# Performance work log

Measured on AMD Instinct MI355X. Metric: run time of the kernel, lower is better.

The kernel has to match this reference:

```python
import jax, jax.numpy as jnp
import numpy as np

SR = 16000
NYQ = SR / 2.0
N_FFT = 400
HOP = 160
WIN = 400
OUT_CHANNELS = 64
OUTPUT_SIZE = 64
MIN_LOW_HZ = 50.0
MIN_BAND_HZ = 50.0
FRAME_LENGTH = 400
EPS_LN = 1e-5


def _to_mel(hz):
    return 2595.0 * np.log10(1.0 + hz / 700.0)


def _to_hz(mel):
    return 700.0 * (10.0 ** (mel / 2595.0) - 1.0)


def setup_inputs() -> dict:
    key = jax.random.key(0)
    k1, = jax.random.split(key, 1)
    waveforms = jax.random.normal(k1, (1024, 1, 16000), dtype=jnp.float32)
    # mel-spaced init, exactly as in __init__ (freq_init='mel', range_constraint=False)
    low_hz = 30.0
    high_hz = NYQ - (MIN_LOW_HZ + MIN_BAND_HZ)
    mel = np.linspace(_to_mel(low_hz), _to_mel(high_hz), OUT_CHANNELS + 1)
    hz = _to_hz(mel)
    low_hz_ = jnp.asarray(hz[:-1], dtype=jnp.float32).reshape(-1, 1)
    band_hz_ = jnp.asarray(np.diff(hz), dtype=jnp.float32).reshape(-1, 1)
    ln_weight = jnp.ones((OUT_CHANNELS, 1), dtype=jnp.float32)
    ln_bias = jnp.zeros((OUT_CHANNELS, 1), dtype=jnp.float32)
    return {
        "waveforms": waveforms,
        "low_hz_": low_hz_,
        "band_hz_": band_hz_,
        "ln_weight": ln_weight,
        "ln_bias": ln_bias,
    }


def _hann_periodic(n):
    # torch.hann_window default: periodic=True
    k = jnp.arange(n, dtype=jnp.float32)
    return 0.5 - 0.5 * jnp.cos(2.0 * jnp.pi * k / n)


def _stft_mag(x):
    pad = N_FFT // 2
    xp = jnp.pad(x, ((0, 0), (pad, pad)), mode="reflect")
    n_frames = 1 + (xp.shape[1] - N_FFT) // HOP
    idx = jnp.arange(n_frames)[:, None] * HOP + jnp.arange(N_FFT)[None, :]
    frames = xp[:, idx] * _hann_periodic(WIN)  # [B, F_t, n_fft]
    spec = jnp.fft.rfft(frames, axis=-1)       # [B, F_t, n_fft//2+1]
    return jnp.abs(spec).transpose(0, 2, 1)    # [B, n_fft//2+1, F_t]


def _get_filters(low_hz_, band_hz_):
    # vectorized over all channels (original loops per channel)
    low = MIN_LOW_HZ + jnp.abs(low_hz_)                                   # [C,1]
    high = jnp.clip(low + MIN_BAND_HZ + jnp.abs(band_hz_), MIN_LOW_HZ, NYQ)
    freq = jnp.linspace(0.0, NYQ, N_FFT // 2 + 1, dtype=jnp.float32)      # [F]
    mask = (freq >= low) & (freq <= high)                                 # [C,F]
    center = (low + high) / 2.0
    bw = high - low
    resp = 1.0 - jnp.abs(freq - center) / (bw / 2.0)                      # triangular
    return jnp.where(mask, resp, 0.0)                                     # [C,F]


def _gln(x, weight, bias):
    # GlobalLayerNorm over dims (1,2) of [B,C,T]
    mean = jnp.mean(x, axis=(1, 2), keepdims=True)
    var = jnp.mean((x - mean) ** 2, axis=(1, 2), keepdims=True)
    return weight * (x - mean) / jnp.sqrt(var + EPS_LN) + bias


def _interp_linear(x, out_size):
    # torch F.interpolate(mode='linear', align_corners=False) along last dim
    t_in = x.shape[-1]
    scale = t_in / out_size
    pos = (jnp.arange(out_size, dtype=jnp.float32) + 0.5) * scale - 0.5
    pos = jnp.clip(pos, 0.0, t_in - 1)
    i0 = jnp.floor(pos).astype(jnp.int32)
    i1 = jnp.minimum(i0 + 1, t_in - 1)
    w = (pos - i0.astype(jnp.float32))
    return x[..., i0] * (1.0 - w) + x[..., i1] * w


def reference(waveforms, low_hz_, band_hz_, ln_weight, ln_bias):
    B = waveforms.shape[0]
    target_length = HOP * (OUTPUT_SIZE - 1) + FRAME_LENGTH  # 10480
    cur = waveforms.shape[-1]
    x = waveforms[:, 0, :]
    if target_length > cur:  # static shape decision
        x = jnp.pad(x, ((0, 0), (0, target_length - cur)))
    mag_spec = _stft_mag(x)                       # [B, 201, F_t]
    filters = _get_filters(low_hz_, band_hz_)     # [C, 201]
    filtered = jnp.einsum("cf,bft->bct", filters, mag_spec)  # [B, C, F_t]
    filtered = _gln(filtered, ln_weight, ln_bias)
    energy = filtered ** 2
    log_energy = jnp.log10(energy + 1e-6)         # [B, C, F_t]
    if log_energy.shape[-1] != OUTPUT_SIZE:
        log_energy = _interp_linear(log_energy, OUTPUT_SIZE)  # [B, C, 64]
    log_energy = log_energy[:, None, :, :].transpose(0, 1, 3, 2)  # [B,1,64,C]
    return (log_energy, filters)
```

## Files before the change

kernel.cpp:

```cpp
#include <hip/hip_runtime.h>
#include <math.h>

#define BLOCK 1024
#define MSTR 209

typedef __attribute__((ext_vector_type(8))) short short8;
typedef __attribute__((ext_vector_type(16))) float f32x16;
typedef __attribute__((ext_vector_type(8))) float f32x8;

__device__ inline unsigned short f2bf(float x) {
    unsigned u = __float_as_uint(x);
    unsigned r = u + 0x7fffu + ((u >> 16) & 1u);
    return (unsigned short)(r >> 16);
}

struct ASplit { short8 h, l; };

__device__ inline ASplit splitA_fast(f32x8 v) {
    unsigned h[4], l[4];
    #pragma unroll
    for (int q = 0; q < 4; ++q) {
        unsigned u0 = __float_as_uint(v[2*q]);
        unsigned u1 = __float_as_uint(v[2*q+1]);
        h[q] = __builtin_amdgcn_perm(u1, u0, 0x07060302u);
        float r0 = v[2*q]   - __uint_as_float(u0 & 0xFFFF0000u);
        float r1 = v[2*q+1] - __uint_as_float(u1 & 0xFFFF0000u);
        l[q] = __builtin_amdgcn_perm(__float_as_uint(r1), __float_as_uint(r0), 0x07060302u);
    }
    ASplit r;
    r.h = __builtin_bit_cast(short8, *(uint4*)h);
    r.l = __builtin_bit_cast(short8, *(uint4*)l);
    return r;
}

__device__ inline f32x8 loadA8(const float* __restrict__ x, int i0) {
    f32x8 r;
    if (i0 >= 0 && i0 <= 15992) {
        float4 a0 = *(const float4*)(x + i0);
        float4 a1 = *(const float4*)(x + i0 + 4);
        r[0] = a0.x; r[1] = a0.y; r[2] = a0.z; r[3] = a0.w;
        r[4] = a1.x; r[5] = a1.y; r[6] = a1.z; r[7] = a1.w;
    } else {
        #pragma unroll
        for (int e = 0; e < 8; ++e) {
            int p = i0 + e;
            p = (p < 0) ? -p : p;
            p = (p > 15999) ? (31998 - p) : p;
            r[e] = x[p];
        }
    }
    return r;
}

__device__ inline void filter_params(int c, const float* low_hz_, const float* band_hz_,
                                     float* fctr, float* finv, int* fks, int* fke) {
    float lo = 50.0f + fabsf(low_hz_[c]);
    float hi = lo + 50.0f + fabsf(band_hz_[c]);
    hi = fminf(fmaxf(hi, 50.0f), 8000.0f);
    float ctr = 0.5f * (lo + hi);
    float hbw = 0.5f * (hi - lo);
    int ks = (int)ceilf(lo * 0.025f);
    if (ks < 0) ks = 0;
    while (40.0f * (float)ks < lo) ++ks;
    while (ks > 0 && 40.0f * (float)(ks - 1) >= lo) --ks;
    int ke = (int)floorf(hi * 0.025f);
    if (ke > 200) ke = 200;
    while (40.0f * (float)ke > hi) --ke;
    while (ke < 200 && 40.0f * (float)(ke + 1) <= hi) ++ke;
    fctr[c] = ctr;
    finv[c] = (hbw > 0.0f) ? (1.0f / hbw) : 0.0f;
    fks[c]  = ks;
    fke[c]  = ke;
}

__global__ void fse_filters(const float* __restrict__ low_hz_,
                            const float* __restrict__ band_hz_,
                            float* __restrict__ out)
{
    int idx = blockIdx.x * 256 + threadIdx.x;
    if (idx >= 64 * 201) return;
    int c = idx / 201;
    int k = idx - c * 201;
    float lo = 50.0f + fabsf(low_hz_[c]);
    float hi = lo + 50.0f + fabsf(band_hz_[c]);
    hi = fminf(fmaxf(hi, 50.0f), 8000.0f);
    float ctr = 0.5f * (lo + hi);
    float hbw = 0.5f * (hi - lo);
    float fq = 40.0f * (float)k;
    float resp = 1.0f - fabsf(fq - ctr) / hbw;
    out[idx] = (fq >= lo && fq <= hi) ? resp : 0.0f;
}

__global__ void fse_setup_B(unsigned short* __restrict__ bt)
{
    int idx = blockIdx.x * 256 + threadIdx.x;
    if (idx >= 372736) return;
    int e   = idx & 7;
    int t   = idx >> 3;
    int row = t % 448;
    int q   = t / 448;
    int p   = q & 3;
    int pl  = (q >> 2) & 1;
    int kc  = q >> 3;
    int n   = kc * 32 + p * 8 + e;
    float v = 0.0f;
    if (n < 400) {
        int bin = -1, isim = 0;
        if (row <= 200) bin = row;
        else if (row >= 224 && row <= 424) { bin = row - 224; isim = 1; }
        if (bin >= 0) {
            int a = (bin * n) % 400;
            float th = 6.283185307179586f * ((float)a / 400.0f);
            float sn, cs;
            sincosf(th, &sn, &cs);
            float wn = 0.5f - 0.5f * cosf(6.283185307179586f * ((float)n / 400.0f));
            v = isim ? (-wn * sn) : (wn * cs);
        }
    }
    unsigned short h = f2bf(v);
    float hf = __uint_as_float((unsigned)h << 16);
    unsigned short l = f2bf(v - hf);
    bt[idx] = pl ? l : h;
}

#define KSTEP(KC, CUROFF, A0c, A1c, A0n, A1n, PRE)                            \
  {                                                                           \
    asm volatile("s_waitcnt vmcnt(0)" ::: "memory");                          \
    __builtin_amdgcn_s_barrier();                                             \
    __builtin_amdgcn_sched_barrier(0);                                        \
    if (PRE) {                                                                \
      A0n = loadA8(x, ab + ((KC) + 1) * 32);                                  \
      A1n = loadA8(x, ab + ((KC) + 1) * 32 + 16);                             \
      const uint4* _src = btg + ((KC) + 1) * 3584;                            \
      const int _bufo = (CUROFF) ^ 57344;                                     \
      _Pragma("unroll")                                                       \
      for (int _i = 0; _i < 4; ++_i) {                                        \
        int _idx = _i * 1024 + tid;                                           \
        if (_idx < 3584) {                                                    \
          __builtin_amdgcn_global_load_lds(                                   \
              (const __attribute__((address_space(1))) unsigned*)(_src + _idx), \
              (__attribute__((address_space(3))) unsigned*)(smem + _bufo + _idx * 16), \
              16, 0, 0);                                                      \
        }                                                                     \
      }                                                                       \
    }                                                                         \
    ASplit _S0 = splitA_fast(A0c);                                            \
    ASplit _S1 = splitA_fast(A1c);                                            \
    const unsigned short* _bs = (const unsigned short*)(smem + (CUROFF));     \
    _Pragma("unroll")                                                         \
    for (int _s = 0; _s < 2; ++_s) {                                          \
      const short8 _Ah = _s ? _S1.h : _S0.h;                                  \
      const short8 _Al = _s ? _S1.l : _S0.l;                                  \
      const int _part = _s * 2 + g;                                           \
      const int _bhof = _part * 3584;                                         \
      const int _blof = (4 + _part) * 3584;                                   \
      _Pragma("unroll")                                                       \
      for (int _i2 = 0; _i2 < 2; ++_i2) {                                     \
        if (_i2 < cnt) {                                                      \
          const int _p = pbase + _i2;                                         \
          const int _roR = _p * 32 + jrow;                                    \
          const int _roI = (_p + 7) * 32 + jrow;                              \
          short8 _BhR = *(const short8*)(_bs + _bhof + _roR * 8);             \
          short8 _BlR = *(const short8*)(_bs + _blof + _roR * 8);             \
          short8 _BhI = *(const short8*)(_bs + _bhof + _roI * 8);             \
          short8 _BlI = *(const short8*)(_bs + _blof + _roI * 8);             \
          accR[_i2] = __builtin_amdgcn_mfma_f32_32x32x16_bf16(_Ah, _BhR, accR[_i2], 0, 0, 0); \
          accR[_i2] = __builtin_amdgcn_mfma_f32_32x32x16_bf16(_Ah, _BlR, accR[_i2], 0, 0, 0); \
          accR[_i2] = __builtin_amdgcn_mfma_f32_32x32x16_bf16(_Al, _BhR, accR[_i2], 0, 0, 0); \
          accI[_i2] = __builtin_amdgcn_mfma_f32_32x32x16_bf16(_Ah, _BhI, accI[_i2], 0, 0, 0); \
          accI[_i2] = __builtin_amdgcn_mfma_f32_32x32x16_bf16(_Ah, _BlI, accI[_i2], 0, 0, 0); \
          accI[_i2] = __builtin_amdgcn_mfma_f32_32x32x16_bf16(_Al, _BhI, accI[_i2], 0, 0, 0); \
        }                                                                     \
      }                                                                       \
    }                                                                         \
    asm volatile("s_waitcnt lgkmcnt(0)" ::: "memory");                        \
    __builtin_amdgcn_sched_barrier(0);                                        \
  }

__global__ __launch_bounds__(1024, 4)
void fse_main(const float* __restrict__ wav,
              const float* __restrict__ low_hz_,
              const float* __restrict__ band_hz_,
              const float* __restrict__ ln_w,
              const float* __restrict__ ln_b,
              const unsigned short* __restrict__ Bt,
              float* __restrict__ out)
{
    __shared__ __align__(16) char smem[114688];
    float* mags = (float*)smem;
    float* fbuf = (float*)(smem + 84544);

    __shared__ float fctr[64], finv[64];
    __shared__ int   fks[64], fke[64];
    __shared__ float red[32];
    __shared__ float stats[2];

    const int b    = blockIdx.x;
    const int tid  = threadIdx.x;
    const int w    = tid >> 6;
    const int lane = tid & 63;
    const float* __restrict__ x = wav + b * 16000;

    if (tid < 64) filter_params(tid, low_hz_, band_hz_, fctr, finv, fks, fke);

    const int mt    = w >> 2;
    const int pq    = w & 3;
    const int pbase = pq * 2;
    const int cnt   = (pq < 3) ? 2 : 1;
    const int jrow  = lane & 31;
    const int g     = lane >> 5;

    const int arow = 32 * mt + jrow;
    const int te   = (arow <= 100) ? arow : 50;
    const int ab   = 160 * te - 200 + g * 8;

    const uint4* __restrict__ btg = (const uint4*)Bt;

    f32x8 aE0 = loadA8(x, ab);
    f32x8 aE1 = loadA8(x, ab + 16);
    f32x8 aO0, aO1;
    {
        #pragma unroll
        for (int i = 0; i < 4; ++i) {
            int idx = i * 1024 + tid;
            if (idx < 3584) {
                __builtin_amdgcn_global_load_lds(
                    (const __attribute__((address_space(1))) unsigned*)(btg + idx),
                    (__attribute__((address_space(3))) unsigned*)(smem + idx * 16),
                    16, 0, 0);
            }
        }
    }

    f32x16 accR[2], accI[2];
    #pragma unroll
    for (int i = 0; i < 2; ++i)
        #pragma unroll
        for (int e = 0; e < 16; ++e) { accR[i][e] = 0.0f; accI[i][e] = 0.0f; }

    KSTEP(0,  0,     aE0, aE1, aO0, aO1, true)
    KSTEP(1,  57344, aO0, aO1, aE0, aE1, true)
    KSTEP(2,  0,     aE0, aE1, aO0, aO1, true)
    KSTEP(3,  57344, aO0, aO1, aE0, aE1, true)
    KSTEP(4,  0,     aE0, aE1, aO0, aO1, true)
    KSTEP(5,  57344, aO0, aO1, aE0, aE1, true)
    KSTEP(6,  0,     aE0, aE1, aO0, aO1, true)
    KSTEP(7,  57344, aO0, aO1, aE0, aE1, true)
    KSTEP(8,  0,     aE0, aE1, aO0, aO1, true)
    KSTEP(9,  57344, aO0, aO1, aE0, aE1, true)
    KSTEP(10, 0,     aE0, aE1, aO0, aO1, true)
    KSTEP(11, 57344, aO0, aO1, aE0, aE1, true)
    KSTEP(12, 0,     aE0, aE1, aO0, aO1, false)

    __syncthreads();

    #pragma unroll
    for (int i = 0; i < 2; ++i) {
        if (i < cnt) {
            const int k = (pbase + i) * 32 + jrow;
            if (k <= 200) {
                #pragma unroll
                for (int r = 0; r < 16; ++r) {
                    int t = 32 * mt + (r & 3) + 8 * (r >> 2) + 4 * g;
                    if (t <= 100) {
                        float re = accR[i][r];
                        float im = accI[i][r];
                        mags[t * MSTR + k] = sqrtf(re * re + im * im);
                    }
                }
            }
        }
    }
    __syncthreads();

    {
        const int t0 = lane;
        const int t1v = 64 + lane;
        const int t1 = (t1v <= 100) ? t1v : 100;
        #pragma unroll
        for (int i = 0; i < 4; ++i) {
            const int c = w * 4 + i;
            const float ctr = fctr[c];
            const float inv = finv[c];
            const int ks = fks[c], ke = fke[c];
            float a0 = 0.0f, a1 = 0.0f;
            for (int k = ks; k <= ke; ++k) {
                float resp = 1.0f - fabsf(40.0f * (float)k - ctr) * inv;
                a0 = fmaf(resp, mags[t0 * MSTR + k], a0);
                a1 = fmaf(resp, mags[t1 * MSTR + k], a1);
            }
            fbuf[c * 101 + t0] = a0;
            if (t1v <= 100) fbuf[c * 101 + t1v] = a1;
        }
    }
    __syncthreads();

    float s = 0.0f, ss = 0.0f;
    for (int i = tid; i < 6464; i += BLOCK) {
        float vv = fbuf[i];
        s += vv;
        ss = fmaf(vv, vv, ss);
    }
    #pragma unroll
    for (int off = 32; off > 0; off >>= 1) {
        s  += __shfl_down(s,  off, 64);
        ss += __shfl_down(ss, off, 64);
    }
    if (lane == 0) { red[w] = s; red[16 + w] = ss; }
    __syncthreads();
    if (tid == 0) {
        float ts = 0.0f, tss = 0.0f;
        for (int i = 0; i < 16; ++i) { ts += red[i]; tss += red[16 + i]; }
        float mu = ts * (1.0f / 6464.0f);
        stats[0] = mu;
        stats[1] = tss * (1.0f / 6464.0f) - mu * mu;
    }
    __syncthreads();
    const float mu   = stats[0];
    const float isig = 1.0f / sqrtf(stats[1] + 1e-5f);

    for (int idx = tid; idx < 4096; idx += BLOCK) {
        const int to = idx >> 6;
        const int c  = idx & 63;
        float pos = ((float)to + 0.5f) * 1.578125f - 0.5f;
        pos = fminf(fmaxf(pos, 0.0f), 100.0f);
        int i0 = (int)floorf(pos);
        int i1 = i0 + 1; if (i1 > 100) i1 = 100;
        float fr = pos - (float)i0;
        float wc = ln_w[c], bc = ln_b[c];
        float x0 = fbuf[c * 101 + i0];
        float x1 = fbuf[c * 101 + i1];
        float y0 = fmaf(wc, (x0 - mu) * isig, bc);
        float y1 = fmaf(wc, (x1 - mu) * isig, bc);
        float l0 = log10f(fmaf(y0, y0, 1e-6f));
        float l1 = log10f(fmaf(y1, y1, 1e-6f));
        out[b * 4096 + idx] = l0 * (1.0f - fr) + l1 * fr;
    }
}

extern "C" void kernel_launch(void* const* d_in, const int* in_sizes, int n_in,
                              void* d_out, int out_size, void* d_ws, size_t ws_size,
                              hipStream_t stream)
{
    const float* wav = (const float*)d_in[0];
    const float* lo  = (const float*)d_in[1];
    const float* bd  = (const float*)d_in[2];
    const float* lw  = (const float*)d_in[3];
    const float* lb  = (const float*)d_in[4];
    float* out = (float*)d_out;

    fse_filters<<<(64 * 201 + 255) / 256, 256, 0, stream>>>(lo, bd, out + 1024 * 4096);

    unsigned short* Bts = (unsigned short*)d_ws;
    fse_setup_B<<<(372736 + 255) / 256, 256, 0, stream>>>(Bts);
    fse_main<<<1024, BLOCK, 0, stream>>>(wav, lo, bd, lw, lb, Bts, out);
}
```

Measured before the change: 213.9 us.

## Remap MFMA waves so each wave reuses B fragments across two M-tiles

Changes the wave-to-tile mapping in the STFT matmul so each wave owns one frequency tile across two time tiles, reusing each LDS B fragment load for two accumulators. One of eight waves idles during the matmul. A loads now happen in-step instead of being prefetched a step ahead. The filterbank loop is vectorized with float4 LDS reads over a 4-aligned padded row stride, and the padding columns are zeroed with a clamped response. This trades less LDS read traffic for more exposed global A-load latency and an idle wave.

```diff
diff --git a/kernel.cpp b/kernel.cpp
--- a/kernel.cpp
+++ b/kernel.cpp
@@ -2,7 +2,7 @@
 #include <math.h>
 
 #define BLOCK 1024
-#define MSTR 209
+#define MSTR 212
 
 typedef __attribute__((ext_vector_type(8))) short short8;
 typedef __attribute__((ext_vector_type(16))) float f32x16;
@@ -123,14 +123,19 @@
     bt[idx] = pl ? l : h;
 }
 
-#define KSTEP(KC, CUROFF, A0c, A1c, A0n, A1n, PRE)                            \
+#define KSTEP(KC, CUROFF, PRE)                                                \
   {                                                                           \
     asm volatile("s_waitcnt vmcnt(0)" ::: "memory");                          \
     __builtin_amdgcn_s_barrier();                                             \
     __builtin_amdgcn_sched_barrier(0);                                        \
+    f32x8 a00, a01, a10, a11;                                                 \
+    if (act) {                                                                \
+      a00 = loadA8(x, ab0 + (KC) * 32);                                       \
+      a01 = loadA8(x, ab0 + (KC) * 32 + 16);                                  \
+      a10 = loadA8(x, ab1 + (KC) * 32);                                       \
+      a11 = loadA8(x, ab1 + (KC) * 32 + 16);                                  \
+    }                                                                         \
     if (PRE) {                                                                \
-      A0n = loadA8(x, ab + ((KC) + 1) * 32);                                  \
-      A1n = loadA8(x, ab + ((KC) + 1) * 32 + 16);                             \
       const uint4* _src = btg + ((KC) + 1) * 3584;                            \
       const int _bufo = (CUROFF) ^ 57344;                                     \
       _Pragma("unroll")                                                       \
@@ -144,33 +149,37 @@
         }                                                                     \
       }                                                                       \
     }                                                                         \
-    ASplit _S0 = splitA_fast(A0c);                                            \
-    ASplit _S1 = splitA_fast(A1c);                                            \
-    const unsigned short* _bs = (const unsigned short*)(smem + (CUROFF));     \
-    _Pragma("unroll")                                                         \
-    for (int _s = 0; _s < 2; ++_s) {                                          \
-      const short8 _Ah = _s ? _S1.h : _S0.h;                                  \
-      const short8 _Al = _s ? _S1.l : _S0.l;                                  \
-      const int _part = _s * 2 + g;                                           \
-      const int _bhof = _part * 3584;                                         \
-      const int _blof = (4 + _part) * 3584;                                   \
+    if (act) {                                                                \
+      ASplit S00 = splitA_fast(a00);                                          \
+      ASplit S01 = splitA_fast(a01);                                          \
+      ASplit S10 = splitA_fast(a10);                                          \
+      ASplit S11 = splitA_fast(a11);                                          \
+      const unsigned short* _bs = (const unsigned short*)(smem + (CUROFF));   \
       _Pragma("unroll")                                                       \
-      for (int _i2 = 0; _i2 < 2; ++_i2) {                                     \
-        if (_i2 < cnt) {                                                      \
-          const int _p = pbase + _i2;                                         \
-          const int _roR = _p * 32 + jrow;                                    \
-          const int _roI = (_p + 7) * 32 + jrow;                              \
-          short8 _BhR = *(const short8*)(_bs + _bhof + _roR * 8);             \
-          short8 _BlR = *(const short8*)(_bs + _blof + _roR * 8);             \
-          short8 _BhI = *(const short8*)(_bs + _bhof + _roI * 8);             \
-          short8 _BlI = *(const short8*)(_bs + _blof + _roI * 8);             \
-          accR[_i2] = __builtin_amdgcn_mfma_f32_32x32x16_bf16(_Ah, _BhR, accR[_i2], 0, 0, 0); \
-          accR[_i2] = __builtin_amdgcn_mfma_f32_32x32x16_bf16(_Ah, _BlR, accR[_i2], 0, 0, 0); \
-          accR[_i2] = __builtin_amdgcn_mfma_f32_32x32x16_bf16(_Al, _BhR, accR[_i2], 0, 0, 0); \
-          accI[_i2] = __builtin_amdgcn_mfma_f32_32x32x16_bf16(_Ah, _BhI, accI[_i2], 0, 0, 0); \
-          accI[_i2] = __builtin_amdgcn_mfma_f32_32x32x16_bf16(_Ah, _BlI, accI[_i2], 0, 0, 0); \
-          accI[_i2] = __builtin_amdgcn_mfma_f32_32x32x16_bf16(_Al, _BhI, accI[_i2], 0, 0, 0); \
-        }                                                                     \
+      for (int _s = 0; _s < 2; ++_s) {                                        \
+        const short8 _Ah0 = _s ? S01.h : S00.h;                               \
+        const short8 _Al0 = _s ? S01.l : S00.l;                               \
+        const short8 _Ah1 = _s ? S11.h : S10.h;                               \
+        const short8 _Al1 = _s ? S11.l : S10.l;                               \
+        const int _part = _s * 2 + g;                                         \
+        const int _bhof = _part * 3584;                                       \
+        const int _blof = (4 + _part) * 3584;                                 \
+        short8 _BhR = *(const short8*)(_bs + _bhof + roR * 8);                \
+        short8 _BlR = *(const short8*)(_bs + _blof + roR * 8);                \
+        short8 _BhI = *(const short8*)(_bs + _bhof + roI * 8);                \
+        short8 _BlI = *(const short8*)(_bs + _blof + roI * 8);                \
+        accR[0] = __builtin_amdgcn_mfma_f32_32x32x16_bf16(_Ah0, _BhR, accR[0], 0, 0, 0); \
+        accR[0] = __builtin_amdgcn_mfma_f32_32x32x16_bf16(_Ah0, _BlR, accR[0], 0, 0, 0); \
+        accR[0] = __builtin_amdgcn_mfma_f32_32x32x16_bf16(_Al0, _BhR, accR[0], 0, 0, 0); \
+        accR[1] = __builtin_amdgcn_mfma_f32_32x32x16_bf16(_Ah1, _BhR, accR[1], 0, 0, 0); \
+        accR[1] = __builtin_amdgcn_mfma_f32_32x32x16_bf16(_Ah1, _BlR, accR[1], 0, 0, 0); \
+        accR[1] = __builtin_amdgcn_mfma_f32_32x32x16_bf16(_Al1, _BhR, accR[1], 0, 0, 0); \
+        accI[0] = __builtin_amdgcn_mfma_f32_32x32x16_bf16(_Ah0, _BhI, accI[0], 0, 0, 0); \
+        accI[0] = __builtin_amdgcn_mfma_f32_32x32x16_bf16(_Ah0, _BlI, accI[0], 0, 0, 0); \
+        accI[0] = __builtin_amdgcn_mfma_f32_32x32x16_bf16(_Al0, _BhI, accI[0], 0, 0, 0); \
+        accI[1] = __builtin_amdgcn_mfma_f32_32x32x16_bf16(_Ah1, _BhI, accI[1], 0, 0, 0); \
+        accI[1] = __builtin_amdgcn_mfma_f32_32x32x16_bf16(_Ah1, _BlI, accI[1], 0, 0, 0); \
+        accI[1] = __builtin_amdgcn_mfma_f32_32x32x16_bf16(_Al1, _BhI, accI[1], 0, 0, 0); \
       }                                                                       \
     }                                                                         \
     asm volatile("s_waitcnt lgkmcnt(0)" ::: "memory");                        \
@@ -188,7 +197,7 @@
 {
     __shared__ __align__(16) char smem[114688];
     float* mags = (float*)smem;
-    float* fbuf = (float*)(smem + 84544);
+    float* fbuf = (float*)(smem + 85648);
 
     __shared__ float fctr[64], finv[64];
     __shared__ int   fks[64], fke[64];
@@ -203,22 +212,23 @@
 
     if (tid < 64) filter_params(tid, low_hz_, band_hz_, fctr, finv, fks, fke);
 
-    const int mt    = w >> 2;
-    const int pq    = w & 3;
-    const int pbase = pq * 2;
-    const int cnt   = (pq < 3) ? 2 : 1;
-    const int jrow  = lane & 31;
-    const int g     = lane >> 5;
-
-    const int arow = 32 * mt + jrow;
-    const int te   = (arow <= 100) ? arow : 50;
-    const int ab   = 160 * te - 200 + g * 8;
+    const int mg   = w >> 3;
+    const int pg   = w & 7;
+    const bool act = (pg < 7);
+    const int jrow = lane & 31;
+    const int g    = lane >> 5;
+    const int roR  = pg * 32 + jrow;
+    const int roI  = (pg + 7) * 32 + jrow;
+
+    const int arow0 = 64 * mg + jrow;
+    const int arow1 = 64 * mg + 32 + jrow;
+    const int te0   = (arow0 <= 100) ? arow0 : 50;
+    const int te1   = (arow1 <= 100) ? arow1 : 50;
+    const int ab0   = 160 * te0 - 200 + g * 8;
+    const int ab1   = 160 * te1 - 200 + g * 8;
 
     const uint4* __restrict__ btg = (const uint4*)Bt;
 
-    f32x8 aE0 = loadA8(x, ab);
-    f32x8 aE1 = loadA8(x, ab + 16);
-    f32x8 aO0, aO1;
     {
         #pragma unroll
         for (int i = 0; i < 4; ++i) {
@@ -238,37 +248,43 @@
         #pragma unroll
         for (int e = 0; e < 16; ++e) { accR[i][e] = 0.0f; accI[i][e] = 0.0f; }
 
-    KSTEP(0,  0,     aE0, aE1, aO0, aO1, true)
-    KSTEP(1,  57344, aO0, aO1, aE0, aE1, true)
-    KSTEP(2,  0,     aE0, aE1, aO0, aO1, true)
-    KSTEP(3,  57344, aO0, aO1, aE0, aE1, true)
-    KSTEP(4,  0,     aE0, aE1, aO0, aO1, true)
-    KSTEP(5,  57344, aO0, aO1, aE0, aE1, true)
-    KSTEP(6,  0,     aE0, aE1, aO0, aO1, true)
-    KSTEP(7,  57344, aO0, aO1, aE0, aE1, true)
-    KSTEP(8,  0,     aE0, aE1, aO0, aO1, true)
-    KSTEP(9,  57344, aO0, aO1, aE0, aE1, true)
-    KSTEP(10, 0,     aE0, aE1, aO0, aO1, true)
-    KSTEP(11, 57344, aO0, aO1, aE0, aE1, true)
-    KSTEP(12, 0,     aE0, aE1, aO0, aO1, false)
-
-    __syncthreads();
-
-    #pragma unroll
-    for (int i = 0; i < 2; ++i) {
-        if (i < cnt) {
-            const int k = (pbase + i) * 32 + jrow;
-            if (k <= 200) {
+    KSTEP(0,  0,     true)
+    KSTEP(1,  57344, true)
+    KSTEP(2,  0,     true)
+    KSTEP(3,  57344, true)
+    KSTEP(4,  0,     true)
+    KSTEP(5,  57344, true)
+    KSTEP(6,  0,     true)
+    KSTEP(7,  57344, true)
+    KSTEP(8,  0,     true)
+    KSTEP(9,  57344, true)
+    KSTEP(10, 0,     true)
+    KSTEP(11, 57344, true)
+    KSTEP(12, 0,     false)
+
+    __syncthreads();
+
+    if (act) {
+        const int k = pg * 32 + jrow;
+        if (k <= 200) {
+            #pragma unroll
+            for (int mtl = 0; mtl < 2; ++mtl) {
                 #pragma unroll
                 for (int r = 0; r < 16; ++r) {
-                    int t = 32 * mt + (r & 3) + 8 * (r >> 2) + 4 * g;
+                    int t = 64 * mg + 32 * mtl + (r & 3) + 8 * (r >> 2) + 4 * g;
                     if (t <= 100) {
-                        float re = accR[i][r];
-                        float im = accI[i][r];
+                        float re = accR[mtl][r];
+                        float im = accI[mtl][r];
                         mags[t * MSTR + k] = sqrtf(re * re + im * im);
                     }
                 }
             }
+        }
+    } else {
+        const int t = 64 * mg + lane;
+        if (t <= 100) {
+            #pragma unroll
+            for (int kk = 201; kk < 212; ++kk) mags[t * MSTR + kk] = 0.0f;
         }
     }
     __syncthreads();
@@ -282,12 +298,20 @@
             const int c = w * 4 + i;
             const float ctr = fctr[c];
             const float inv = finv[c];
-            const int ks = fks[c], ke = fke[c];
+            const int ks4 = fks[c] & ~3;
+            const int ke  = fke[c];
             float a0 = 0.0f, a1 = 0.0f;
-            for (int k = ks; k <= ke; ++k) {
-                float resp = 1.0f - fabsf(40.0f * (float)k - ctr) * inv;
-                a0 = fmaf(resp, mags[t0 * MSTR + k], a0);
-                a1 = fmaf(resp, mags[t1 * MSTR + k], a1);
+            for (int k4 = ks4; k4 <= ke; k4 += 4) {
+                float4 m0 = *(const float4*)&mags[t0 * MSTR + k4];
+                float4 m1 = *(const float4*)&mags[t1 * MSTR + k4];
+                #pragma unroll
+                for (int j = 0; j < 4; ++j) {
+                    float resp = fmaxf(1.0f - fabsf(40.0f * (float)(k4 + j) - ctr) * inv, 0.0f);
+                    float mj0 = (j == 0) ? m0.x : (j == 1) ? m0.y : (j == 2) ? m0.z : m0.w;
+                    float mj1 = (j == 0) ? m1.x : (j == 1) ? m1.y : (j == 2) ? m1.z : m1.w;
+                    a0 = fmaf(resp, mj0, a0);
+                    a1 = fmaf(resp, mj1, a1);
+                }
             }
             fbuf[c * 101 + t0] = a0;
             if (t1v <= 100) fbuf[c * 101 + t1v] = a1;
```

Result: slower. 534.3 us (+149.7%).
